# Optimization experiments

Measured on AMD Instinct MI355X. Metric: run time of the kernel, lower is better.

The kernel has to match this reference:

```python
import jax, jax.numpy as jnp
import numpy as np

# Constants derived from init_kwargs (nuScenes occupancy setup)
XYZ_MIN = jnp.array([-40.0, -40.0, -1.0], dtype=jnp.float32)
XYZ_MAX = jnp.array([40.0, 40.0, 5.4], dtype=jnp.float32)
STEPSIZE = 0.5
_ext = np.array([80.0, 80.0, 6.4])
VOXEL_SIZE = float((_ext.prod() / (200 * 200 * 16)) ** (1.0 / 3.0))  # = 0.4
N_SAMPLES = int(np.linalg.norm(np.array([100, 100, 8]) + 1) / STEPSIZE) + 1  # 287


def trilinear_sample(grid, pts):
    """grid: (C, Dx, Dy, Dz) laid out as [C, x, y, z]; pts: (M, 3) world xyz -> (M, C).
    Matches torch F.grid_sample(align_corners=True) after the coord flip in grid_sampler:
    normalized coord u in [0,1] maps to index u*(dim-1)."""
    C, Dx, Dy, Dz = grid.shape
    dims = jnp.array([Dx, Dy, Dz], dtype=pts.dtype)
    u = (pts - XYZ_MIN) / (XYZ_MAX - XYZ_MIN)
    idx = jnp.clip(u * (dims - 1.0), 0.0, dims - 1.0)  # out-of-bbox pts are masked later
    i0 = jnp.clip(jnp.floor(idx), 0.0, dims - 2.0).astype(jnp.int32)
    w = idx - i0  # (M, 3) in [0, 1]
    flat = grid.reshape(C, -1)
    out = jnp.zeros((C, pts.shape[0]), dtype=pts.dtype)
    for ox in (0, 1):
        wx = w[:, 0] if ox else 1.0 - w[:, 0]
        for oy in (0, 1):
            wy = w[:, 1] if oy else 1.0 - w[:, 1]
            for oz in (0, 1):
                wz = w[:, 2] if oz else 1.0 - w[:, 2]
                lin = ((i0[:, 0] + ox) * Dy + (i0[:, 1] + oy)) * Dz + (i0[:, 2] + oz)
                out = out + jnp.take(flat, lin, axis=1) * (wx * wy * wz)
    return out.T


def _forward(rays_o, rays_d, voxel, rgb_recon):
    ro = rays_o.reshape(-1, 3)
    rd = rays_d.reshape(-1, 3)
    R = ro.shape[0]
    # test-mode sampling: rng = arange(N_samples), Zval = stepsize * voxel_size * rng
    zval = (STEPSIZE * VOXEL_SIZE) * jnp.arange(N_SAMPLES, dtype=ro.dtype)  # (N,)
    pts = ro[:, None, :] + rd[:, None, :] * zval[None, :, None]  # (R, N, 3)
    inside = jnp.all((pts >= XYZ_MIN) & (pts <= XYZ_MAX), axis=-1)  # ~mask_outbbox, (R, N)
    flat_pts = pts.reshape(-1, 3)
    # density sigmoid -> 'prob' compositing
    dens = trilinear_sample(voxel, flat_pts).reshape(R, N_SAMPLES)
    sig = jax.nn.sigmoid(dens)
    # probs = 0 outside bbox; last sample forced to 1 unless inside (then overwritten by sig)
    probs = jnp.where(inside, sig, 0.0)
    probs = probs.at[:, -1].set(jnp.where(inside[:, -1], sig[:, -1], 1.0))
    cum = jnp.minimum(jnp.cumsum(probs, axis=1), 1.0)  # cumsum.clamp(max=1)
    probs = jnp.diff(cum, axis=1, prepend=jnp.zeros((R, 1), cum.dtype))
    depth = jnp.sum(probs * zval[None, :], axis=-1)  # (R,)
    # rgb rendering (img_recon_head=True)
    rgb = trilinear_sample(rgb_recon, flat_pts).reshape(R, N_SAMPLES, 3)
    rgb = jnp.where(inside[..., None], rgb, 0.0)
    rgb_marched = jnp.sum(probs[..., None] * rgb, axis=-2)  # (R, 3)
    return depth, rgb_marched


def setup_inputs() -> dict:
    key = jax.random.key(0)
    k1, k2, k3, k4 = jax.random.split(key, 4)
    num_cam, H, W = 6, 90, 160
    # camera origins near the scene center, inside the bbox
    rays_o = (jax.random.uniform(k1, (num_cam, H, W, 3), jnp.float32) - 0.5) \
        * jnp.array([4.0, 4.0, 1.0], jnp.float32) + jnp.array([0.0, 0.0, 1.5], jnp.float32)
    d = jax.random.normal(k2, (num_cam, H, W, 3), jnp.float32)
    rays_d = d / jnp.linalg.norm(d, axis=-1, keepdims=True)
    voxel = jax.random.normal(k3, (1, 200, 200, 16), jnp.float32)
    rgb_recon = jax.random.uniform(k4, (3, 200, 200, 16), jnp.float32)
    return {"rays_o": rays_o, "rays_d": rays_d, "voxel": voxel, "rgb_recon": rgb_recon}


def reference(rays_o, rays_d, voxel, rgb_recon):
    return _forward(rays_o, rays_d, voxel, rgb_recon)
```

## Files before the change

kernel.cpp:

```cpp
#include <hip/hip_runtime.h>
#include <hip/hip_bf16.h>


namespace {
constexpr int DX = 200, DY = 200, DZ = 16;
constexpr int GRID_N = DX * DY * DZ;
constexpr int NS = 287;
constexpr float ZSTEP = 0.2f;
}

extern "C" __global__ void __launch_bounds__(256)
nerf_march_kernel(const float* __restrict__ ro,
                  const float* __restrict__ rd,
                  const float* __restrict__ vox,
                  const float* __restrict__ rgbg,
                  float* __restrict__ out, int R)
{
    const int r = blockIdx.x * blockDim.x + threadIdx.x;
    if (r >= R) return;

    const float ox = ro[3 * r + 0];
    const float oy = ro[3 * r + 1];
    const float oz = ro[3 * r + 2];
    const float dx = rd[3 * r + 0];
    const float dy = rd[3 * r + 1];
    const float dz = rd[3 * r + 2];

    float c = 0.0f;
    float depth = 0.0f;
    float a0 = 0.0f, a1 = 0.0f, a2 = 0.0f;
    const float zlast = ZSTEP * (float)(NS - 1);

    #pragma unroll 1
    for (int n = 0; n < NS; ++n) {
        const float z  = ZSTEP * (float)n;
        const float px = ox + dx * z;
        const float py = oy + dy * z;
        const float pz = oz + dz * z;

        const bool inside = (px >= -40.0f) & (px <= 40.0f) &
                            (py >= -40.0f) & (py <= 40.0f) &
                            (pz >= -1.0f)  & (pz <= 5.4f);
        if (!inside) {
            if (c < 1.0f) depth += (1.0f - c) * zlast;
            break;
        }

        float fx = fminf(fmaxf((px + 40.0f) / 80.0f * 199.0f, 0.0f), 199.0f);
        float fy = fminf(fmaxf((py + 40.0f) / 80.0f * 199.0f, 0.0f), 199.0f);
        float fz = fminf(fmaxf((pz + 1.0f)  / 6.4f  * 15.0f,  0.0f), 15.0f);
        int ix = min((int)fx, DX - 2);
        int iy = min((int)fy, DY - 2);
        int iz = min((int)fz, DZ - 2);
        const float wx = fx - (float)ix, wy = fy - (float)iy, wz = fz - (float)iz;
        const float ux = 1.0f - wx, uy = 1.0f - wy, uz = 1.0f - wz;

        const float w000 = ux * uy * uz, w001 = ux * uy * wz;
        const float w010 = ux * wy * uz, w011 = ux * wy * wz;
        const float w100 = wx * uy * uz, w101 = wx * uy * wz;
        const float w110 = wx * wy * uz, w111 = wx * wy * wz;

        const int base = (ix * DY + iy) * DZ + iz;
        const int SX = DY * DZ;
        const int SY = DZ;

        const float dens =
            vox[base]           * w000 + vox[base + 1]           * w001 +
            vox[base + SY]      * w010 + vox[base + SY + 1]      * w011 +
            vox[base + SX]      * w100 + vox[base + SX + 1]      * w101 +
            vox[base + SX + SY] * w110 + vox[base + SX + SY + 1] * w111;

        const float sig = 1.0f / (1.0f + __expf(-dens));

        const float newc = c + sig;
        const float p = fminf(newc, 1.0f) - fminf(c, 1.0f);

        depth += p * z;

        #pragma unroll
        for (int ch = 0; ch < 3; ++ch) {
            const float* g = rgbg + ch * GRID_N;
            const float v =
                g[base]           * w000 + g[base + 1]           * w001 +
                g[base + SY]      * w010 + g[base + SY + 1]      * w011 +
                g[base + SX]      * w100 + g[base + SX + 1]      * w101 +
                g[base + SX + SY] * w110 + g[base + SX + SY + 1] * w111;
            if (ch == 0) a0 += p * v;
            else if (ch == 1) a1 += p * v;
            else a2 += p * v;
        }

        c = newc;
        if (c >= 1.0f) break;
    }

    out[r]             = depth;
    out[R + 3 * r]     = a0;
    out[R + 3 * r + 1] = a1;
    out[R + 3 * r + 2] = a2;
}

extern "C" void kernel_launch(void* const* d_in, const int* in_sizes, int n_in,
                              void* d_out, int out_size, void* d_ws, size_t ws_size,
                              hipStream_t stream) {
    const float* ro   = (const float*)d_in[0];
    const float* rd   = (const float*)d_in[1];
    const float* vox  = (const float*)d_in[2];
    const float* rgbg = (const float*)d_in[3];
    float* out = (float*)d_out;

    const int R = in_sizes[0] / 3;
    const int block = 256;
    const int grid = (R + block - 1) / block;

    nerf_march_kernel<<<grid, block, 0, stream>>>(ro, rd, vox, rgbg, out, R);
}
```

Measured before the change: 71.88 us.

## Repack density and RGB grids into interleaved float4 and shrink march blocks

Adds a pre-pass kernel that interleaves the density grid and the three RGB channel grids into one float4 array in workspace. The march kernel then does eight 16-byte gathers per sample instead of 32 scalar gathers spread over four separate arrays. The block size drops from 256 to 64 to spread the 8640 rays over more CUs, and divisions are folded into constant multipliers. The cost is an extra full-grid repack pass each call, about 10 MB written and read, plus a second launch.

After: 74.99 us. 1.04x slower.

```diff
diff --git a/kernel.cpp b/kernel.cpp
--- a/kernel.cpp
+++ b/kernel.cpp
@@ -1,5 +1,4 @@
 #include <hip/hip_runtime.h>
-#include <hip/hip_bf16.h>
 
 
 namespace {
@@ -10,10 +9,19 @@
 }
 
 extern "C" __global__ void __launch_bounds__(256)
+nerf_repack_kernel(const float* __restrict__ vox,
+                   const float* __restrict__ rgbg,
+                   float4* __restrict__ packed)
+{
+    const int i = blockIdx.x * blockDim.x + threadIdx.x;
+    if (i >= GRID_N) return;
+    packed[i] = make_float4(vox[i], rgbg[i], rgbg[GRID_N + i], rgbg[2 * GRID_N + i]);
+}
+
+extern "C" __global__ void __launch_bounds__(64)
 nerf_march_kernel(const float* __restrict__ ro,
                   const float* __restrict__ rd,
-                  const float* __restrict__ vox,
-                  const float* __restrict__ rgbg,
+                  const float4* __restrict__ g4,
                   float* __restrict__ out, int R)
 {
     const int r = blockIdx.x * blockDim.x + threadIdx.x;
@@ -46,9 +54,9 @@
             break;
         }
 
-        float fx = fminf(fmaxf((px + 40.0f) / 80.0f * 199.0f, 0.0f), 199.0f);
-        float fy = fminf(fmaxf((py + 40.0f) / 80.0f * 199.0f, 0.0f), 199.0f);
-        float fz = fminf(fmaxf((pz + 1.0f)  / 6.4f  * 15.0f,  0.0f), 15.0f);
+        float fx = fminf(fmaxf((px + 40.0f) * 2.4875f,  0.0f), 199.0f);
+        float fy = fminf(fmaxf((py + 40.0f) * 2.4875f,  0.0f), 199.0f);
+        float fz = fminf(fmaxf((pz + 1.0f)  * 2.34375f, 0.0f), 15.0f);
         int ix = min((int)fx, DX - 2);
         int iy = min((int)fy, DY - 2);
         int iz = min((int)fz, DZ - 2);
@@ -60,35 +68,34 @@
         const float w100 = wx * uy * uz, w101 = wx * uy * wz;
         const float w110 = wx * wy * uz, w111 = wx * wy * wz;
 
-        const int base = (ix * DY + iy) * DZ + iz;
         const int SX = DY * DZ;
         const int SY = DZ;
+        const int base = (ix * DY + iy) * DZ + iz;
+
+        const float4 q000 = g4[base];
+        const float4 q001 = g4[base + 1];
+        const float4 q010 = g4[base + SY];
+        const float4 q011 = g4[base + SY + 1];
+        const float4 q100 = g4[base + SX];
+        const float4 q101 = g4[base + SX + 1];
+        const float4 q110 = g4[base + SX + SY];
+        const float4 q111 = g4[base + SX + SY + 1];
 
         const float dens =
-            vox[base]           * w000 + vox[base + 1]           * w001 +
-            vox[base + SY]      * w010 + vox[base + SY + 1]      * w011 +
-            vox[base + SX]      * w100 + vox[base + SX + 1]      * w101 +
-            vox[base + SX + SY] * w110 + vox[base + SX + SY + 1] * w111;
+            q000.x * w000 + q001.x * w001 + q010.x * w010 + q011.x * w011 +
+            q100.x * w100 + q101.x * w101 + q110.x * w110 + q111.x * w111;
 
         const float sig = 1.0f / (1.0f + __expf(-dens));
-
         const float newc = c + sig;
         const float p = fminf(newc, 1.0f) - fminf(c, 1.0f);
 
         depth += p * z;
-
-        #pragma unroll
-        for (int ch = 0; ch < 3; ++ch) {
-            const float* g = rgbg + ch * GRID_N;
-            const float v =
-                g[base]           * w000 + g[base + 1]           * w001 +
-                g[base + SY]      * w010 + g[base + SY + 1]      * w011 +
-                g[base + SX]      * w100 + g[base + SX + 1]      * w101 +
-                g[base + SX + SY] * w110 + g[base + SX + SY + 1] * w111;
-            if (ch == 0) a0 += p * v;
-            else if (ch == 1) a1 += p * v;
-            else a2 += p * v;
-        }
+        a0 += p * (q000.y * w000 + q001.y * w001 + q010.y * w010 + q011.y * w011 +
+                   q100.y * w100 + q101.y * w101 + q110.y * w110 + q111.y * w111);
+        a1 += p * (q000.z * w000 + q001.z * w001 + q010.z * w010 + q011.z * w011 +
+                   q100.z * w100 + q101.z * w101 + q110.z * w110 + q111.z * w111);
+        a2 += p * (q000.w * w000 + q001.w * w001 + q010.w * w010 + q011.w * w011 +
+                   q100.w * w100 + q101.w * w101 + q110.w * w110 + q111.w * w111);
 
         c = newc;
         if (c >= 1.0f) break;
@@ -108,10 +115,10 @@
     const float* vox  = (const float*)d_in[2];
     const float* rgbg = (const float*)d_in[3];
     float* out = (float*)d_out;
+    float4* packed = (float4*)d_ws;
 
     const int R = in_sizes[0] / 3;
-    const int block = 256;
-    const int grid = (R + block - 1) / block;
 
-    nerf_march_kernel<<<grid, block, 0, stream>>>(ro, rd, vox, rgbg, out, R);
+    nerf_repack_kernel<<<(GRID_N + 255) / 256, 256, 0, stream>>>(vox, rgbg, packed);
+    nerf_march_kernel<<<(R + 63) / 64, 64, 0, stream>>>(ro, rd, packed, out, R);
 }
```

## Split each ray across eight lanes, one per trilinear corner, reduce via shuffles

Applied to the files above, without the earlier changes.

Each ray is now handled by eight threads, each fetching one trilinear corner for density and the three RGB channels, and the corner contributions are summed with xor shuffles. This raises parallelism from 8640 threads to eight times as many and spreads the 32 gathers per step across lanes to hide latency. The per-step address math, sigmoid and compositing are repeated in all eight lanes, and only four lanes write outputs. The divisions are also folded into constant multipliers, which may change rounding slightly.

Result: slower. 75.47 us (+5.0%).

```diff
diff --git a/kernel.cpp b/kernel.cpp
--- a/kernel.cpp
+++ b/kernel.cpp
@@ -1,5 +1,4 @@
 #include <hip/hip_runtime.h>
-#include <hip/hip_bf16.h>
 
 
 namespace {
@@ -10,21 +9,26 @@
 }
 
 extern "C" __global__ void __launch_bounds__(256)
-nerf_march_kernel(const float* __restrict__ ro,
-                  const float* __restrict__ rd,
-                  const float* __restrict__ vox,
-                  const float* __restrict__ rgbg,
-                  float* __restrict__ out, int R)
+nerf_march8_kernel(const float* __restrict__ ro,
+                   const float* __restrict__ rd,
+                   const float* __restrict__ vox,
+                   const float* __restrict__ rgbg,
+                   float* __restrict__ out, int R)
 {
-    const int r = blockIdx.x * blockDim.x + threadIdx.x;
-    if (r >= R) return;
+    const int tid = blockIdx.x * blockDim.x + threadIdx.x;
+    const int ray = tid >> 3;
+    if (ray >= R) return;
+    const int corner = tid & 7;
+    const int cx = (corner >> 2) & 1;
+    const int cy = (corner >> 1) & 1;
+    const int cz = corner & 1;
 
-    const float ox = ro[3 * r + 0];
-    const float oy = ro[3 * r + 1];
-    const float oz = ro[3 * r + 2];
-    const float dx = rd[3 * r + 0];
-    const float dy = rd[3 * r + 1];
-    const float dz = rd[3 * r + 2];
+    const float ox = ro[3 * ray + 0];
+    const float oy = ro[3 * ray + 1];
+    const float oz = ro[3 * ray + 2];
+    const float dx = rd[3 * ray + 0];
+    const float dy = rd[3 * ray + 1];
+    const float dz = rd[3 * ray + 2];
 
     float c = 0.0f;
     float depth = 0.0f;
@@ -46,58 +50,51 @@
             break;
         }
 
-        float fx = fminf(fmaxf((px + 40.0f) / 80.0f * 199.0f, 0.0f), 199.0f);
-        float fy = fminf(fmaxf((py + 40.0f) / 80.0f * 199.0f, 0.0f), 199.0f);
-        float fz = fminf(fmaxf((pz + 1.0f)  / 6.4f  * 15.0f,  0.0f), 15.0f);
-        int ix = min((int)fx, DX - 2);
-        int iy = min((int)fy, DY - 2);
-        int iz = min((int)fz, DZ - 2);
+        float fx = fminf(fmaxf((px + 40.0f) * 2.4875f,  0.0f), 199.0f);
+        float fy = fminf(fmaxf((py + 40.0f) * 2.4875f,  0.0f), 199.0f);
+        float fz = fminf(fmaxf((pz + 1.0f)  * 2.34375f, 0.0f), 15.0f);
+        const int ix = min((int)fx, DX - 2);
+        const int iy = min((int)fy, DY - 2);
+        const int iz = min((int)fz, DZ - 2);
         const float wx = fx - (float)ix, wy = fy - (float)iy, wz = fz - (float)iz;
-        const float ux = 1.0f - wx, uy = 1.0f - wy, uz = 1.0f - wz;
 
-        const float w000 = ux * uy * uz, w001 = ux * uy * wz;
-        const float w010 = ux * wy * uz, w011 = ux * wy * wz;
-        const float w100 = wx * uy * uz, w101 = wx * uy * wz;
-        const float w110 = wx * wy * uz, w111 = wx * wy * wz;
+        const float wcx = cx ? wx : 1.0f - wx;
+        const float wcy = cy ? wy : 1.0f - wy;
+        const float wcz = cz ? wz : 1.0f - wz;
+        const float wc  = wcx * wcy * wcz;
+        const int idx = ((ix + cx) * DY + (iy + cy)) * DZ + (iz + cz);
 
-        const int base = (ix * DY + iy) * DZ + iz;
-        const int SX = DY * DZ;
-        const int SY = DZ;
+        float vd = vox[idx]               * wc;
+        float v0 = rgbg[idx]              * wc;
+        float v1 = rgbg[idx + GRID_N]     * wc;
+        float v2 = rgbg[idx + 2 * GRID_N] * wc;
 
-        const float dens =
-            vox[base]           * w000 + vox[base + 1]           * w001 +
-            vox[base + SY]      * w010 + vox[base + SY + 1]      * w011 +
-            vox[base + SX]      * w100 + vox[base + SX + 1]      * w101 +
-            vox[base + SX + SY] * w110 + vox[base + SX + SY + 1] * w111;
+        #pragma unroll
+        for (int m = 1; m <= 4; m <<= 1) {
+            vd += __shfl_xor(vd, m, 64);
+            v0 += __shfl_xor(v0, m, 64);
+            v1 += __shfl_xor(v1, m, 64);
+            v2 += __shfl_xor(v2, m, 64);
+        }
 
-        const float sig = 1.0f / (1.0f + __expf(-dens));
-
+        const float sig = 1.0f / (1.0f + __expf(-vd));
         const float newc = c + sig;
         const float p = fminf(newc, 1.0f) - fminf(c, 1.0f);
 
         depth += p * z;
-
-        #pragma unroll
-        for (int ch = 0; ch < 3; ++ch) {
-            const float* g = rgbg + ch * GRID_N;
-            const float v =
-                g[base]           * w000 + g[base + 1]           * w001 +
-                g[base + SY]      * w010 + g[base + SY + 1]      * w011 +
-                g[base + SX]      * w100 + g[base + SX + 1]      * w101 +
-                g[base + SX + SY] * w110 + g[base + SX + SY + 1] * w111;
-            if (ch == 0) a0 += p * v;
-            else if (ch == 1) a1 += p * v;
-            else a2 += p * v;
-        }
+        a0 += p * v0;
+        a1 += p * v1;
+        a2 += p * v2;
 
         c = newc;
         if (c >= 1.0f) break;
     }
 
-    out[r]             = depth;
-    out[R + 3 * r]     = a0;
-    out[R + 3 * r + 1] = a1;
-    out[R + 3 * r + 2] = a2;
+    if (corner < 4) {
+        const float v = (corner == 0) ? depth : (corner == 1) ? a0 : (corner == 2) ? a1 : a2;
+        const int addr = (corner == 0) ? ray : (R + 3 * ray + (corner - 1));
+        out[addr] = v;
+    }
 }
 
 extern "C" void kernel_launch(void* const* d_in, const int* in_sizes, int n_in,
@@ -110,8 +107,9 @@
     float* out = (float*)d_out;
 
     const int R = in_sizes[0] / 3;
+    const int threads = R * 8;
     const int block = 256;
-    const int grid = (R + block - 1) / block;
+    const int grid = (threads + block - 1) / block;
 
-    nerf_march_kernel<<<grid, block, 0, stream>>>(ro, rd, vox, rgbg, out, R);
+    nerf_march8_kernel<<<grid, block, 0, stream>>>(ro, rd, vox, rgbg, out, R);
 }
```
